# Kernel tuning notes

Hardware: AMD Instinct MI355X
Metric: run time of the kernel (lower is better)

Reference implementation:

```python
import jax, jax.numpy as jnp
import numpy as np

B, N, D, H = 8, 1025, 768, 12
PRE = 1            # prefix (CLS) tokens
P = N - PRE        # patch tokens
HD = D // H
EPS = 1e-6


def setup_inputs() -> dict:
    key = jax.random.key(0)
    ks = jax.random.split(key, 8)
    x = jax.random.normal(ks[0], (B, N, D), dtype=jnp.float32)
    graph = jax.random.uniform(ks[1], (B, P, P), dtype=jnp.float32)
    transferability = jax.random.uniform(ks[2], (B, P), dtype=jnp.float32)
    Wqkv = jax.random.normal(ks[3], (3 * D, D), dtype=jnp.float32) * 0.02
    bqkv = jnp.zeros((3 * D,), dtype=jnp.float32)
    Wproj = jax.random.normal(ks[4], (D, D), dtype=jnp.float32) * 0.02
    bproj = jnp.zeros((D,), dtype=jnp.float32)
    return {"x": x, "graph": graph, "transferability": transferability,
            "Wqkv": Wqkv, "bqkv": bqkv, "Wproj": Wproj, "bproj": bproj,
            "prefix_tokens": PRE}


def _build_mask(graph, transferability, prefix_tokens, n_tokens):
    # patch_weights: [B, P]
    pw = transferability / (jnp.sum(transferability, axis=1, keepdims=True) + EPS)
    b, p = pw.shape
    pre = prefix_tokens
    # Block layout: [[1s (pre,pre), pw broadcast (pre,P)], [pw[:,None] (P,pre), graph]]
    top_left = jnp.ones((b, pre, pre), dtype=graph.dtype)
    top_right = jnp.broadcast_to(pw[:, None, :], (b, pre, p))
    bot_left = jnp.broadcast_to(pw[:, :, None], (b, p, pre))
    top = jnp.concatenate([top_left, top_right], axis=2)
    bot = jnp.concatenate([bot_left, graph], axis=2)
    return jnp.concatenate([top, bot], axis=1)  # [B, N, N]


def reference(x, graph, transferability, Wqkv, bqkv, Wproj, bproj, prefix_tokens):
    bsz, n, d = x.shape
    scale = HD ** -0.5
    qkv = x @ Wqkv.T + bqkv                          # [B, N, 3D]
    qkv = qkv.reshape(bsz, n, 3, H, HD).transpose(2, 0, 3, 1, 4)  # [3, B, H, N, hd]
    q, k, v = qkv[0], qkv[1], qkv[2]
    attn = jax.nn.softmax(jnp.einsum('bhid,bhjd->bhij', q, k) * scale, axis=-1)
    mask = _build_mask(graph, transferability, prefix_tokens, n)  # [B, N, N]
    attn = attn * mask[:, None, :, :]
    attn = attn / (jnp.sum(attn, axis=-1, keepdims=True) + EPS)
    out = jnp.einsum('bhij,bhjd->bhid', attn, v)     # [B, H, N, hd]
    out = out.transpose(0, 2, 1, 3).reshape(bsz, n, d)
    return out @ Wproj.T + bproj
```

## Files before the change

### kernel.cpp

```cpp
#include <hip/hip_runtime.h>
#include <stdint.h>

constexpr int Bq = 8, Nn = 1025, Dd = 768, Hh = 12, HDd = 64, Pp = 1024;
constexpr int NP = 1088;
constexpr int MROWS = Bq * Nn;
constexpr float EPSI = 1e-6f;

typedef __attribute__((ext_vector_type(8))) short bfrag;
typedef __attribute__((ext_vector_type(4))) float ffrag;
typedef __attribute__((ext_vector_type(4))) float f4;
typedef __attribute__((ext_vector_type(4))) unsigned short us4;

#define MFMA16(a, b, c) __builtin_amdgcn_mfma_f32_16x16x32_bf16((a), (b), (c), 0, 0, 0)

#if __has_builtin(__builtin_amdgcn_exp2f)
#define EXP2(x) __builtin_amdgcn_exp2f(x)
#else
#define EXP2(x) exp2f(x)
#endif

__device__ __forceinline__ unsigned short f2bf(float f) {
  union { float f; uint32_t u; } v{f};
  uint32_t u = v.u;
  return (unsigned short)((u + 0x7fffu + ((u >> 16) & 1u)) >> 16);
}
__device__ __forceinline__ float bf2f(unsigned short s) {
  union { uint32_t u; float f; } v; v.u = ((uint32_t)s) << 16; return v.f;
}
__device__ __forceinline__ uint32_t pkbf(float a, float b) {
  uint32_t r;
  asm("v_cvt_pk_bf16_f32 %0, %1, %2" : "=v"(r) : "v"(a), "v"(b));
  return r;
}

__device__ __forceinline__ void gload16(const void* g, void* l) {
  __builtin_amdgcn_global_load_lds((const __attribute__((address_space(1))) unsigned int*)g,
                                   (__attribute__((address_space(3))) unsigned int*)l, 16, 0, 0);
}

__global__ __launch_bounds__(256) void conv_kernel(const float* __restrict__ src,
                                                   unsigned short* __restrict__ dst, int n4) {
  int idx = blockIdx.x * blockDim.x + threadIdx.x;
  int stride = gridDim.x * blockDim.x;
  for (int i = idx; i < n4; i += stride) {
    f4 v = ((const f4*)src)[i];
    us4 o; o[0] = f2bf(v[0]); o[1] = f2bf(v[1]); o[2] = f2bf(v[2]); o[3] = f2bf(v[3]);
    ((us4*)dst)[i] = o;
  }
}

__global__ __launch_bounds__(256) void pw_kernel(const float* __restrict__ tr, float* __restrict__ pw) {
  int b = blockIdx.x;
  __shared__ float red[256];
  float s = 0.f;
  for (int j = threadIdx.x; j < Pp; j += 256) s += tr[b * Pp + j];
  red[threadIdx.x] = s; __syncthreads();
  for (int o = 128; o > 0; o >>= 1) { if (threadIdx.x < o) red[threadIdx.x] += red[threadIdx.x + o]; __syncthreads(); }
  float inv = 1.f / (red[0] + EPSI);
  for (int j = threadIdx.x; j < Pp; j += 256) pw[b * Pp + j] = tr[b * Pp + j] * inv;
}

__global__ __launch_bounds__(256) void mask_kernel(const float* __restrict__ graph,
                                                   const float* __restrict__ pw,
                                                   unsigned short* __restrict__ mask) {
  int i = blockIdx.x, b = blockIdx.y;
  unsigned short* mrow = mask + ((size_t)b * NP + i) * NP;
  if (i >= Nn) { for (int j = threadIdx.x; j < NP; j += 256) mrow[j] = 0; return; }
  if (i == 0) {
    for (int j = threadIdx.x; j < NP; j += 256) {
      float v = (j == 0) ? 1.f : (j <= Pp ? pw[b * Pp + j - 1] : 0.f);
      mrow[j] = f2bf(v);
    }
  } else {
    const float* grow = graph + ((size_t)b * Pp + (i - 1)) * Pp;
    for (int j = threadIdx.x; j < NP; j += 256) {
      float v = (j == 0) ? pw[b * Pp + i - 1] : (j <= Pp ? grow[j - 1] : 0.f);
      mrow[j] = f2bf(v);
    }
  }
}

__global__ __launch_bounds__(256) void padzero_kernel(unsigned short* __restrict__ Qo,
                                                      unsigned short* __restrict__ Ko,
                                                      unsigned short* __restrict__ Vo) {
  int bh = blockIdx.x;
  unsigned short* qp = Qo + ((size_t)bh * NP + Nn) * 64;
  unsigned short* kp = Ko + ((size_t)bh * NP + Nn) * 64;
  for (int idx = threadIdx.x; idx < (NP - Nn) * 64; idx += 256) { qp[idx] = 0; kp[idx] = 0; }
  unsigned short* vp = Vo + (size_t)bh * 64 * NP;
  for (int idx = threadIdx.x; idx < 64 * (NP - Nn); idx += 256) {
    int d = idx / (NP - Nn), j = Nn + (idx - d * (NP - Nn));
    vp[(size_t)d * NP + j] = 0;
  }
}

__device__ __forceinline__ void gemm_main(const unsigned short* __restrict__ A, int rowA0, int rowAmax,
                                          const unsigned short* __restrict__ Bw, int rowB0,
                                          uint4* lds, ffrag acc[4][4], int tid) {
  const int l = tid & 63, lm = l & 15, lg = l >> 4, w = tid >> 6, wr = w >> 1, wc = w & 1;
  const unsigned short* aS[4]; const unsigned short* bS[4];
#pragma unroll
  for (int q = 0; q < 4; q++) {
    int c = tid + 256 * q, r = c >> 3, p = c & 7, g = p ^ (r & 7);
    int ra = rowA0 + r; if (ra > rowAmax) ra = rowAmax;
    aS[q] = A + (size_t)ra * 768 + 8 * g;
    bS[q] = Bw + (size_t)(rowB0 + r) * 768 + 8 * g;
  }
  uint4* buf0 = lds;
  uint4* buf1 = lds + 2048;
#pragma unroll
  for (int q = 0; q < 4; q++) {
    gload16(aS[q], buf0 + tid + 256 * q);
    gload16(bS[q], buf0 + 1024 + tid + 256 * q);
    aS[q] += 64; bS[q] += 64;
  }
  asm volatile("s_waitcnt vmcnt(0)" ::: "memory");
  __builtin_amdgcn_sched_barrier(0);
  __builtin_amdgcn_s_barrier();
#pragma unroll 1
  for (int kt = 0; kt < 12; kt++) {
    uint4* cur = (kt & 1) ? buf1 : buf0;
    uint4* nxt = (kt & 1) ? buf0 : buf1;
    if (kt < 11) {
#pragma unroll
      for (int q = 0; q < 4; q++) {
        gload16(aS[q], nxt + tid + 256 * q);
        gload16(bS[q], nxt + 1024 + tid + 256 * q);
        aS[q] += 64; bS[q] += 64;
      }
    }
    const bfrag* LA = (const bfrag*)cur;
    const bfrag* LB = (const bfrag*)(cur + 1024);
    bfrag af[4][2], bf_[4][2];
#pragma unroll
    for (int am = 0; am < 4; am++) {
      int row = wr * 64 + am * 16 + lm;
      af[am][0] = LA[row * 8 + ((0 + lg) ^ (row & 7))];
      af[am][1] = LA[row * 8 + ((4 + lg) ^ (row & 7))];
    }
#pragma unroll
    for (int an = 0; an < 4; an++) {
      int row = wc * 64 + an * 16 + lm;
      bf_[an][0] = LB[row * 8 + ((0 + lg) ^ (row & 7))];
      bf_[an][1] = LB[row * 8 + ((4 + lg) ^ (row & 7))];
    }
#pragma unroll
    for (int am = 0; am < 4; am++)
#pragma unroll
      for (int an = 0; an < 4; an++) {
        acc[am][an] = MFMA16(af[am][0], bf_[an][0], acc[am][an]);
        acc[am][an] = MFMA16(af[am][1], bf_[an][1], acc[am][an]);
      }
    asm volatile("s_waitcnt vmcnt(0)" ::: "memory");
    __builtin_amdgcn_sched_barrier(0);
    __builtin_amdgcn_s_barrier();
  }
}

__device__ __forceinline__ int xcd_chunk_map(int orig, int nwg) {
  int qq = nwg >> 3, rr = nwg & 7;
  int xcd = orig & 7, idx = orig >> 3;
  int base = (xcd < rr) ? xcd * (qq + 1) : rr * (qq + 1) + (xcd - rr) * qq;
  return base + idx;
}

__global__ __launch_bounds__(256) void qkv_gemm_kernel(const unsigned short* __restrict__ X,
                                                       const unsigned short* __restrict__ W,
                                                       const float* __restrict__ bias,
                                                       unsigned short* __restrict__ Qo,
                                                       unsigned short* __restrict__ Ko,
                                                       unsigned short* __restrict__ Vo) {
  __shared__ uint4 lds[4096];
  int tid = threadIdx.x;
  int wg = xcd_chunk_map(blockIdx.x, 65 * 18);
  int xt = wg / 18, yt = wg - 18 * xt;
  ffrag zero4 = {0.f, 0.f, 0.f, 0.f};
  ffrag acc[4][4];
#pragma unroll
  for (int i = 0; i < 4; i++)
#pragma unroll
    for (int j = 0; j < 4; j++) acc[i][j] = zero4;
  gemm_main(X, xt * 128, MROWS - 1, W, yt * 128, lds, acc, tid);
  const int l = tid & 63, lm = l & 15, lg = l >> 4, w = tid >> 6, wr = w >> 1, wc = w & 1;
#pragma unroll
  for (int an = 0; an < 4; an++) {
    int gc = yt * 128 + wc * 64 + an * 16 + lm;
    int which = gc / 768, rr = gc - which * 768, h = rr >> 6, hd = rr & 63;
    float bv = bias[gc];
#pragma unroll
    for (int am = 0; am < 4; am++) {
      int grb = xt * 128 + wr * 64 + am * 16 + 4 * lg;
#pragma unroll
      for (int r = 0; r < 4; r++) {
        int gr = grb + r;
        if (gr >= MROWS) continue;
        int b = gr / Nn, i = gr - b * Nn;
        size_t bh = (size_t)(b * Hh + h);
        float v = acc[am][an][r] + bv;
        if (which == 0)      Qo[(bh * NP + i) * 64 + hd] = f2bf(v * 0.18033688f);
        else if (which == 1) Ko[(bh * NP + i) * 64 + hd] = f2bf(v);
        else                 Vo[(bh * 64 + hd) * NP + i] = f2bf(v);
      }
    }
  }
}

__global__ __launch_bounds__(256) void proj_gemm_kernel(const unsigned short* __restrict__ A,
                                                        const unsigned short* __restrict__ W,
                                                        const float* __restrict__ bias,
                                                        float* __restrict__ out) {
  __shared__ uint4 lds[4096];
  int tid = threadIdx.x;
  int wg = xcd_chunk_map(blockIdx.x, 65 * 6);
  int xt = wg / 6, yt = wg - 6 * xt;
  ffrag zero4 = {0.f, 0.f, 0.f, 0.f};
  ffrag acc[4][4];
#pragma unroll
  for (int i = 0; i < 4; i++)
#pragma unroll
    for (int j = 0; j < 4; j++) acc[i][j] = zero4;
  gemm_main(A, xt * 128, MROWS - 1, W, yt * 128, lds, acc, tid);
  const int l = tid & 63, lm = l & 15, lg = l >> 4, w = tid >> 6, wr = w >> 1, wc = w & 1;
#pragma unroll
  for (int an = 0; an < 4; an++) {
    int gc = yt * 128 + wc * 64 + an * 16 + lm;
    float bv = bias[gc];
#pragma unroll
    for (int am = 0; am < 4; am++) {
      int grb = xt * 128 + wr * 64 + am * 16 + 4 * lg;
#pragma unroll
      for (int r = 0; r < 4; r++) {
        int gr = grb + r;
        if (gr >= MROWS) continue;
        out[(size_t)gr * 768 + gc] = acc[am][an][r] + bv;
      }
    }
  }
}

__global__ __launch_bounds__(256) void attn_kernel(const unsigned short* __restrict__ Qg,
                                                   const unsigned short* __restrict__ Kg,
                                                   const unsigned short* __restrict__ Vg,
                                                   const unsigned short* __restrict__ Mg,
                                                   unsigned short* __restrict__ Og) {
  __shared__ uint4 smem[2560];
  int tid = threadIdx.x, w = tid >> 6, l = tid & 63, lm = l & 15, lg = l >> 4;
  int bx = blockIdx.x;
  int b = bx & 7, t5 = bx >> 3;
  int h = t5 % 12, ib = t5 / 12;
  size_t bh = (size_t)(b * Hh + h);
  const unsigned short* Qb = Qg + bh * NP * 64;
  const unsigned short* Kb = Kg + bh * NP * 64;
  const unsigned short* Vb = Vg + bh * 64 * NP;
  int i0a = ib * 128 + w * 16;
  int i0b = i0a + 64;
  int irowa = i0a + lm; if (irowa > NP - 1) irowa = NP - 1;
  int irowb = i0b + lm; if (irowb > NP - 1) irowb = NP - 1;
  const unsigned short* Mrowa = Mg + (size_t)b * NP * NP + (size_t)irowa * NP;
  const unsigned short* Mrowb = Mg + (size_t)b * NP * NP + (size_t)irowb * NP;

  bfrag qa0 = *(const bfrag*)(Qb + (size_t)irowa * 64 + 8 * lg);
  bfrag qa1 = *(const bfrag*)(Qb + (size_t)irowa * 64 + 32 + 8 * lg);
  bfrag qb0 = *(const bfrag*)(Qb + (size_t)irowb * 64 + 8 * lg);
  bfrag qb1 = *(const bfrag*)(Qb + (size_t)irowb * 64 + 32 + 8 * lg);

  ffrag zero4 = {0.f, 0.f, 0.f, 0.f};
  ffrag oaccA[4] = {zero4, zero4, zero4, zero4};
  ffrag oaccB[4] = {zero4, zero4, zero4, zero4};
  float TpA = 0.f, TpB = 0.f;

  int rS = tid >> 3, pS = tid & 7;
  int rS2 = rS + 32;
  const unsigned short* kS0 = Kb + (size_t)rS * 64 + 8 * (pS ^ (rS & 7));
  const unsigned short* kS1 = Kb + (size_t)rS2 * 64 + 8 * (pS ^ (rS2 & 7));
  const unsigned short* vS0 = Vb + (size_t)rS * NP + 8 * (pS ^ (rS & 7));
  const unsigned short* vS1 = Vb + (size_t)rS2 * NP + 8 * (pS ^ (rS2 & 7));

  char* Pbase = (char*)(smem + 2048) + w * 2048;

  gload16(kS0, smem + tid);
  gload16(kS1, smem + tid + 256);
  gload16(vS0, smem + 512 + tid);
  gload16(vS1, smem + 512 + tid + 256);
  asm volatile("s_waitcnt vmcnt(0)" ::: "memory");
  __builtin_amdgcn_sched_barrier(0);
  __builtin_amdgcn_s_barrier();

#pragma unroll 1
  for (int t = 0; t < 17; t++) {
    int cb = (t & 1) << 10;
    if (t < 16) {
      int nb = ((t + 1) & 1) << 10;
      size_t ko = (size_t)(t + 1) * 4096;
      int vo = (t + 1) * 64;
      gload16(kS0 + ko, smem + nb + tid);
      gload16(kS1 + ko, smem + nb + tid + 256);
      gload16(vS0 + vo, smem + nb + 512 + tid);
      gload16(vS1 + vo, smem + nb + 512 + tid + 256);
    }
    int j0 = t * 64;
    us4 mvA[4], mvB[4];
#pragma unroll
    for (int jm = 0; jm < 4; jm++) {
      mvA[jm] = *(const us4*)(Mrowa + j0 + 16 * jm + 4 * lg);
      mvB[jm] = *(const us4*)(Mrowb + j0 + 16 * jm + 4 * lg);
    }
    const bfrag* LK = (const bfrag*)(smem + cb);
    const bfrag* LV = (const bfrag*)(smem + cb + 512);

    bfrag ka[4], kb2[4];
#pragma unroll
    for (int jm = 0; jm < 4; jm++) {
      int row = jm * 16 + lm;
      ka[jm]  = LK[row * 8 + ((0 + lg) ^ (row & 7))];
      kb2[jm] = LK[row * 8 + ((4 + lg) ^ (row & 7))];
    }
    ffrag sa[4], sb[4];
    __builtin_amdgcn_s_setprio(1);
#pragma unroll
    for (int jm = 0; jm < 4; jm++) {
      ffrag a = zero4;
      a = MFMA16(ka[jm], qa0, a);
      a = MFMA16(kb2[jm], qa1, a);
      sa[jm] = a;
      ffrag bb = zero4;
      bb = MFMA16(ka[jm], qb0, bb);
      bb = MFMA16(kb2[jm], qb1, bb);
      sb[jm] = bb;
    }
    __builtin_amdgcn_s_setprio(0);

    bfrag vf[2][4];
#pragma unroll
    for (int ks = 0; ks < 2; ks++)
#pragma unroll
      for (int dm = 0; dm < 4; dm++) {
        int vrow = dm * 16 + lm;
        vf[ks][dm] = LV[vrow * 8 + ((ks * 4 + lg) ^ (vrow & 7))];
      }

#pragma unroll
    for (int jm = 0; jm < 4; jm++) {
      float p0 = EXP2(sa[jm][0]), p1 = EXP2(sa[jm][1]), p2 = EXP2(sa[jm][2]), p3 = EXP2(sa[jm][3]);
      float q0 = p0 * bf2f(mvA[jm][0]), q1 = p1 * bf2f(mvA[jm][1]);
      float q2 = p2 * bf2f(mvA[jm][2]), q3 = p3 * bf2f(mvA[jm][3]);
      TpA += (q0 + q1) + (q2 + q3);
      uint2 pk; pk.x = pkbf(q0, q1); pk.y = pkbf(q2, q3);
      int cpos = (((jm << 1) | (lg >> 1)) ^ (lm & 7));
      *(uint2*)(Pbase + lm * 128 + cpos * 16 + 8 * (lg & 1)) = pk;
    }
    __builtin_amdgcn_s_setprio(1);
#pragma unroll
    for (int ks = 0; ks < 2; ks++) {
      bfrag pa = *(const bfrag*)(Pbase + lm * 128 + ((((ks << 2) | lg)) ^ (lm & 7)) * 16);
#pragma unroll
      for (int dm = 0; dm < 4; dm++) oaccA[dm] = MFMA16(pa, vf[ks][dm], oaccA[dm]);
    }
    __builtin_amdgcn_s_setprio(0);

#pragma unroll
    for (int jm = 0; jm < 4; jm++) {
      float p0 = EXP2(sb[jm][0]), p1 = EXP2(sb[jm][1]), p2 = EXP2(sb[jm][2]), p3 = EXP2(sb[jm][3]);
      float q0 = p0 * bf2f(mvB[jm][0]), q1 = p1 * bf2f(mvB[jm][1]);
      float q2 = p2 * bf2f(mvB[jm][2]), q3 = p3 * bf2f(mvB[jm][3]);
      TpB += (q0 + q1) + (q2 + q3);
      uint2 pk; pk.x = pkbf(q0, q1); pk.y = pkbf(q2, q3);
      int cpos = (((jm << 1) | (lg >> 1)) ^ (lm & 7));
      *(uint2*)(Pbase + lm * 128 + cpos * 16 + 8 * (lg & 1)) = pk;
    }
    __builtin_amdgcn_s_setprio(1);
#pragma unroll
    for (int ks = 0; ks < 2; ks++) {
      bfrag pa = *(const bfrag*)(Pbase + lm * 128 + ((((ks << 2) | lg)) ^ (lm & 7)) * 16);
#pragma unroll
      for (int dm = 0; dm < 4; dm++) oaccB[dm] = MFMA16(pa, vf[ks][dm], oaccB[dm]);
    }
    __builtin_amdgcn_s_setprio(0);

    asm volatile("s_waitcnt vmcnt(0)" ::: "memory");
    __builtin_amdgcn_sched_barrier(0);
    __builtin_amdgcn_s_barrier();
  }
  TpA += __shfl_xor(TpA, 16); TpA += __shfl_xor(TpA, 32);
  TpB += __shfl_xor(TpB, 16); TpB += __shfl_xor(TpB, 32);
  float dnA_row = 1.f / TpA;
  float dnB_row = 1.f / TpB;
  float dnA[4], dnB[4];
#pragma unroll
  for (int r = 0; r < 4; r++) { dnA[r] = __shfl(dnA_row, 4 * lg + r); dnB[r] = __shfl(dnB_row, 4 * lg + r); }
#pragma unroll
  for (int dm = 0; dm < 4; dm++)
#pragma unroll
    for (int r = 0; r < 4; r++) {
      int ia = i0a + 4 * lg + r;
      if (ia < Nn) Og[((size_t)(b * Nn + ia)) * Dd + h * 64 + dm * 16 + lm] = f2bf(oaccA[dm][r] * dnA[r]);
      int ibr = i0b + 4 * lg + r;
      if (ibr < Nn) Og[((size_t)(b * Nn + ibr)) * Dd + h * 64 + dm * 16 + lm] = f2bf(oaccB[dm][r] * dnB[r]);
    }
}

extern "C" void kernel_launch(void* const* d_in, const int* in_sizes, int n_in,
                              void* d_out, int out_size, void* d_ws, size_t ws_size,
                              hipStream_t stream) {
  const float* x      = (const float*)d_in[0];
  const float* graph  = (const float*)d_in[1];
  const float* transf = (const float*)d_in[2];
  const float* Wqkv   = (const float*)d_in[3];
  const float* bqkv   = (const float*)d_in[4];
  const float* Wproj  = (const float*)d_in[5];
  const float* bproj  = (const float*)d_in[6];
  float* out = (float*)d_out;
  char* ws = (char*)d_ws;

  unsigned short* xbf  = (unsigned short*)(ws + 0);
  unsigned short* wqb  = (unsigned short*)(ws + 12595200);
  unsigned short* wpb  = (unsigned short*)(ws + 16134144);
  unsigned short* Qb   = (unsigned short*)(ws + 17313792);
  unsigned short* Kb   = (unsigned short*)(ws + 30683136);
  unsigned short* Vb   = (unsigned short*)(ws + 44052480);
  float*          pw   = (float*)(ws + 57421824);
  unsigned short* mask = (unsigned short*)(ws + 57454592);
  unsigned short* aob  = xbf;

  conv_kernel<<<2048, 256, 0, stream>>>(x, xbf, (MROWS * Dd) / 4);
  conv_kernel<<<1728, 256, 0, stream>>>(Wqkv, wqb, (3 * Dd * Dd) / 4);
  conv_kernel<<<576, 256, 0, stream>>>(Wproj, wpb, (Dd * Dd) / 4);
  pw_kernel<<<Bq, 256, 0, stream>>>(transf, pw);
  mask_kernel<<<dim3(NP, Bq), 256, 0, stream>>>(graph, pw, mask);
  padzero_kernel<<<96, 256, 0, stream>>>(Qb, Kb, Vb);
  qkv_gemm_kernel<<<65 * 18, 256, 0, stream>>>(xbf, wqb, bqkv, Qb, Kb, Vb);
  attn_kernel<<<864, 256, 0, stream>>>(Qb, Kb, Vb, mask, aob);
  proj_gemm_kernel<<<65 * 6, 256, 0, stream>>>(aob, wpb, bproj, out);
}
```

Measured before the change: 209.5 us.

## Halve GEMM K-tile with new LDS layout; separate P buffers in attention

The shared GEMM mainloop now uses a K-tile of 32 instead of 64, which halves LDS per block to 32KB and doubles the iteration count. It also switches to a column-major-by-chunk LDS layout with an XOR row swizzle so each lane does one fragment read per operand. The aim is higher occupancy for the QKV and projection GEMMs, at the cost of more barriers per K. The attention kernel now gives each wave separate P staging buffers for the A and B row halves. Both softmax-probability writes can then finish before the PV MFMAs are issued together, at the cost of more LDS per block.

```diff
diff --git a/kernel.cpp b/kernel.cpp
--- a/kernel.cpp
+++ b/kernel.cpp
@@ -98,59 +98,56 @@
                                           const unsigned short* __restrict__ Bw, int rowB0,
                                           uint4* lds, ffrag acc[4][4], int tid) {
   const int l = tid & 63, lm = l & 15, lg = l >> 4, w = tid >> 6, wr = w >> 1, wc = w & 1;
-  const unsigned short* aS[4]; const unsigned short* bS[4];
-#pragma unroll
-  for (int q = 0; q < 4; q++) {
-    int c = tid + 256 * q, r = c >> 3, p = c & 7, g = p ^ (r & 7);
+  const unsigned short* aS[2]; const unsigned short* bS[2];
+#pragma unroll
+  for (int q = 0; q < 2; q++) {
+    int s = tid + 256 * q;
+    int c = s >> 7, r = (s & 127) ^ (2 * c);
     int ra = rowA0 + r; if (ra > rowAmax) ra = rowAmax;
-    aS[q] = A + (size_t)ra * 768 + 8 * g;
-    bS[q] = Bw + (size_t)(rowB0 + r) * 768 + 8 * g;
+    aS[q] = A + (size_t)ra * 768 + 8 * c;
+    bS[q] = Bw + (size_t)(rowB0 + r) * 768 + 8 * c;
   }
   uint4* buf0 = lds;
-  uint4* buf1 = lds + 2048;
-#pragma unroll
-  for (int q = 0; q < 4; q++) {
+  uint4* buf1 = lds + 1024;
+#pragma unroll
+  for (int q = 0; q < 2; q++) {
     gload16(aS[q], buf0 + tid + 256 * q);
-    gload16(bS[q], buf0 + 1024 + tid + 256 * q);
-    aS[q] += 64; bS[q] += 64;
+    gload16(bS[q], buf0 + 512 + tid + 256 * q);
+    aS[q] += 32; bS[q] += 32;
   }
   asm volatile("s_waitcnt vmcnt(0)" ::: "memory");
   __builtin_amdgcn_sched_barrier(0);
   __builtin_amdgcn_s_barrier();
 #pragma unroll 1
-  for (int kt = 0; kt < 12; kt++) {
+  for (int kt = 0; kt < 24; kt++) {
     uint4* cur = (kt & 1) ? buf1 : buf0;
     uint4* nxt = (kt & 1) ? buf0 : buf1;
-    if (kt < 11) {
-#pragma unroll
-      for (int q = 0; q < 4; q++) {
+    if (kt < 23) {
+#pragma unroll
+      for (int q = 0; q < 2; q++) {
         gload16(aS[q], nxt + tid + 256 * q);
-        gload16(bS[q], nxt + 1024 + tid + 256 * q);
-        aS[q] += 64; bS[q] += 64;
+        gload16(bS[q], nxt + 512 + tid + 256 * q);
+        aS[q] += 32; bS[q] += 32;
       }
     }
     const bfrag* LA = (const bfrag*)cur;
-    const bfrag* LB = (const bfrag*)(cur + 1024);
-    bfrag af[4][2], bf_[4][2];
+    const bfrag* LB = (const bfrag*)(cur + 512);
+    bfrag af[4], bf_[4];
 #pragma unroll
     for (int am = 0; am < 4; am++) {
       int row = wr * 64 + am * 16 + lm;
-      af[am][0] = LA[row * 8 + ((0 + lg) ^ (row & 7))];
-      af[am][1] = LA[row * 8 + ((4 + lg) ^ (row & 7))];
+      af[am] = LA[lg * 128 + (row ^ (2 * lg))];
     }
 #pragma unroll
     for (int an = 0; an < 4; an++) {
       int row = wc * 64 + an * 16 + lm;
-      bf_[an][0] = LB[row * 8 + ((0 + lg) ^ (row & 7))];
-      bf_[an][1] = LB[row * 8 + ((4 + lg) ^ (row & 7))];
+      bf_[an] = LB[lg * 128 + (row ^ (2 * lg))];
     }
 #pragma unroll
     for (int am = 0; am < 4; am++)
 #pragma unroll
-      for (int an = 0; an < 4; an++) {
-        acc[am][an] = MFMA16(af[am][0], bf_[an][0], acc[am][an]);
-        acc[am][an] = MFMA16(af[am][1], bf_[an][1], acc[am][an]);
-      }
+      for (int an = 0; an < 4; an++)
+        acc[am][an] = MFMA16(af[am], bf_[an], acc[am][an]);
     asm volatile("s_waitcnt vmcnt(0)" ::: "memory");
     __builtin_amdgcn_sched_barrier(0);
     __builtin_amdgcn_s_barrier();
@@ -170,7 +167,7 @@
                                                        unsigned short* __restrict__ Qo,
                                                        unsigned short* __restrict__ Ko,
                                                        unsigned short* __restrict__ Vo) {
-  __shared__ uint4 lds[4096];
+  __shared__ uint4 lds[2048];
   int tid = threadIdx.x;
   int wg = xcd_chunk_map(blockIdx.x, 65 * 18);
   int xt = wg / 18, yt = wg - 18 * xt;
@@ -209,7 +206,7 @@
                                                         const unsigned short* __restrict__ W,
                                                         const float* __restrict__ bias,
                                                         float* __restrict__ out) {
-  __shared__ uint4 lds[4096];
+  __shared__ uint4 lds[2048];
   int tid = threadIdx.x;
   int wg = xcd_chunk_map(blockIdx.x, 65 * 6);
   int xt = wg / 6, yt = wg - 6 * xt;
@@ -243,7 +240,7 @@
                                                    const unsigned short* __restrict__ Vg,
                                                    const unsigned short* __restrict__ Mg,
                                                    unsigned short* __restrict__ Og) {
-  __shared__ uint4 smem[2560];
+  __shared__ uint4 smem[3072];
   int tid = threadIdx.x, w = tid >> 6, l = tid & 63, lm = l & 15, lg = l >> 4;
   int bx = blockIdx.x;
   int b = bx & 7, t5 = bx >> 3;
@@ -276,7 +273,8 @@
   const unsigned short* vS0 = Vb + (size_t)rS * NP + 8 * (pS ^ (rS & 7));
   const unsigned short* vS1 = Vb + (size_t)rS2 * NP + 8 * (pS ^ (rS2 & 7));
 
-  char* Pbase = (char*)(smem + 2048) + w * 2048;
+  char* PAbase = (char*)(smem + 2048) + w * 4096;
+  char* PBbase = PAbase + 2048;
 
   gload16(kS0, smem + tid);
   gload16(kS1, smem + tid + 256);
@@ -347,17 +345,8 @@
       TpA += (q0 + q1) + (q2 + q3);
       uint2 pk; pk.x = pkbf(q0, q1); pk.y = pkbf(q2, q3);
       int cpos = (((jm << 1) | (lg >> 1)) ^ (lm & 7));
-      *(uint2*)(Pbase + lm * 128 + cpos * 16 + 8 * (lg & 1)) = pk;
-    }
-    __builtin_amdgcn_s_setprio(1);
-#pragma unroll
-    for (int ks = 0; ks < 2; ks++) {
-      bfrag pa = *(const bfrag*)(Pbase + lm * 128 + ((((ks << 2) | lg)) ^ (lm & 7)) * 16);
-#pragma unroll
-      for (int dm = 0; dm < 4; dm++) oaccA[dm] = MFMA16(pa, vf[ks][dm], oaccA[dm]);
-    }
-    __builtin_amdgcn_s_setprio(0);
-
+      *(uint2*)(PAbase + lm * 128 + cpos * 16 + 8 * (lg & 1)) = pk;
+    }
 #pragma unroll
     for (int jm = 0; jm < 4; jm++) {
       float p0 = EXP2(sb[jm][0]), p1 = EXP2(sb[jm][1]), p2 = EXP2(sb[jm][2]), p3 = EXP2(sb[jm][3]);
@@ -366,14 +355,20 @@
       TpB += (q0 + q1) + (q2 + q3);
       uint2 pk; pk.x = pkbf(q0, q1); pk.y = pkbf(q2, q3);
       int cpos = (((jm << 1) | (lg >> 1)) ^ (lm & 7));
-      *(uint2*)(Pbase + lm * 128 + cpos * 16 + 8 * (lg & 1)) = pk;
+      *(uint2*)(PBbase + lm * 128 + cpos * 16 + 8 * (lg & 1)) = pk;
     }
     __builtin_amdgcn_s_setprio(1);
 #pragma unroll
     for (int ks = 0; ks < 2; ks++) {
-      bfrag pa = *(const bfrag*)(Pbase + lm * 128 + ((((ks << 2) | lg)) ^ (lm & 7)) * 16);
-#pragma unroll
-      for (int dm = 0; dm < 4; dm++) oaccB[dm] = MFMA16(pa, vf[ks][dm], oaccB[dm]);
+      bfrag pa = *(const bfrag*)(PAbase + lm * 128 + ((((ks << 2) | lg)) ^ (lm & 7)) * 16);
+#pragma unroll
+      for (int dm = 0; dm < 4; dm++) oaccA[dm] = MFMA16(pa, vf[ks][dm], oaccA[dm]);
+    }
+#pragma unroll
+    for (int ks = 0; ks < 2; ks++) {
+      bfrag pb = *(const bfrag*)(PBbase + lm * 128 + ((((ks << 2) | lg)) ^ (lm & 7)) * 16);
+#pragma unroll
+      for (int dm = 0; dm < 4; dm++) oaccB[dm] = MFMA16(pb, vf[ks][dm], oaccB[dm]);
     }
     __builtin_amdgcn_s_setprio(0);
 
```

Measured after the change: 243.6 us. 16.3% more time.
